# Kernel optimization log

Hardware: AMD Instinct MI355X
Metric: run time of the kernel (lower is better)

Reference implementation:

```python
import jax, jax.numpy as jnp
import numpy as np
from itertools import permutations

N = 4            # n_streams
C = 2048         # hidden_size
NC = N * C
NFACT = 24       # 4!
DFF = 4 * C
B, S = 2, 4096
EPS = 1.1920929e-07  # torch F.rms_norm default eps = finfo(fp32).eps


def _perm_mat():
    perms = list(permutations(range(N)))
    P = np.zeros((len(perms), N * N), np.float32)
    for i, p in enumerate(perms):
        for r, c in enumerate(p):
            P[i, r * N + c] = 1.0
    return jnp.asarray(P)


def setup_inputs() -> dict:
    key = jax.random.key(0)
    ks = jax.random.split(key, 8)
    total_out = 2 * N + NFACT
    return {
        "x_streams": jax.random.normal(ks[0], (B, S, N, C), jnp.float32),
        "W_all": jax.random.normal(ks[1], (total_out, NC), jnp.float32) * (1.0 / np.sqrt(NC)),
        "b_all": jax.random.normal(ks[2], (total_out,), jnp.float32) * 0.02,
        "alpha_pre": jnp.array([0.01], jnp.float32),
        "alpha_post": jnp.array([0.01], jnp.float32),
        "alpha_res": jnp.array([0.01], jnp.float32),
        "W1": jax.random.normal(ks[3], (DFF, C), jnp.float32) * (1.0 / np.sqrt(C)),
        "b1": jnp.zeros((DFF,), jnp.float32),
        "W2": jax.random.normal(ks[4], (C, DFF), jnp.float32) * (1.0 / np.sqrt(DFF)),
        "b2": jnp.zeros((C,), jnp.float32),
        "perm_mat": _perm_mat(),
    }


def reference(x_streams, W_all, b_all, alpha_pre, alpha_post, alpha_res, W1, b1, W2, b2, perm_mat):
    # --- coefficients: fused RMSNorm + projection + gating ---
    x_flat = x_streams.reshape(*x_streams.shape[:-2], NC)            # (B,S,nC)
    x_norm = x_flat * jax.lax.rsqrt(jnp.mean(x_flat * x_flat, axis=-1, keepdims=True) + EPS)
    all_proj = x_norm @ W_all.T                                       # (B,S,2n+n!)
    pre_proj = all_proj[..., :N]
    post_proj = all_proj[..., N:2 * N]
    res_proj = all_proj[..., 2 * N:]
    h_pre = jax.nn.sigmoid(alpha_pre * pre_proj + b_all[:N])          # (B,S,n)
    h_post = 2.0 * jax.nn.sigmoid(alpha_post * post_proj + b_all[N:2 * N])
    a_res = jax.nn.softmax(alpha_res * res_proj + b_all[2 * N:], axis=-1)  # (B,S,n!)
    H_res = (a_res @ perm_mat).reshape(*a_res.shape[:-1], N, N)       # (B,S,n,n)
    H_merged = H_res - h_post[..., :, None] * h_pre[..., None, :]
    # --- pre-map: weighted sum over streams ---
    layer_input = jnp.einsum('bsn,bsnc->bsc', h_pre, x_streams)       # (B,S,C)
    # --- wrapped layer: GELU MLP (no residual) ---
    h = jax.nn.gelu(layer_input @ W1.T + b1, approximate=False)
    layer_output = h @ W2.T + b2                                      # (B,S,C)
    # --- post-res mixing ---
    out = jnp.einsum('bsij,bsjc->bsic', H_merged, x_streams) \
        + h_post[..., None] * layer_output[..., None, :]
    return out
```

## Files before the change

kernel.cpp:

```cpp
#include <hip/hip_runtime.h>
#include <hip/hip_bf16.h>
#include <math.h>

#define NC_DIM 8192
#define C_DIM 2048
#define NTOK 8192
#define EPS_RMS 1.1920929e-07f

typedef __bf16 bf16_t;
typedef __attribute__((ext_vector_type(8))) __bf16 bf16x8;
typedef __attribute__((ext_vector_type(4))) __bf16 bf16x4;
typedef __attribute__((ext_vector_type(4))) float f32x4;

__device__ __forceinline__ void gload_lds16(const void* g, void* l) {
    __builtin_amdgcn_global_load_lds(
        (const __attribute__((address_space(1))) void*)g,
        (__attribute__((address_space(3))) void*)l, 16, 0, 0);
}

__global__ __launch_bounds__(256) void cvt_f32_bf16(const float* __restrict__ in,
                                                    bf16_t* __restrict__ out,
                                                    const int n4) {
    int i = blockIdx.x * 256 + threadIdx.x;
    const int stride = gridDim.x * 256;
    for (; i < n4; i += stride) {
        f32x4 v = ((const f32x4*)in)[i];
        bf16x4 bv;
        bv.x = (__bf16)v.x; bv.y = (__bf16)v.y; bv.z = (__bf16)v.z; bv.w = (__bf16)v.w;
        ((bf16x4*)out)[i] = bv;
    }
}

__global__ __launch_bounds__(256) void k_proj(
    const float* __restrict__ x,
    const float* __restrict__ Wall,
    const float* __restrict__ ball,
    const float* __restrict__ apre,
    const float* __restrict__ apost,
    const float* __restrict__ ares,
    const float* __restrict__ perm,
    float* __restrict__ hpre_g,
    float* __restrict__ hpost_g,
    float* __restrict__ Hm_g)
{
    __shared__ __align__(16) bf16_t xs[32 * 264];
    __shared__ __align__(16) bf16_t wsl[32 * 264];
    __shared__ float dparts[4][32][32];
    __shared__ float ssq_s[32];
    __shared__ float Ps[384];

    const int t = threadIdx.x;
    const int lane = t & 63;
    const int w = t >> 6;
    const int tok0 = blockIdx.x * 32;

    for (int i = t; i < 384; i += 256) Ps[i] = perm[i];

    const int row = t >> 3;
    const int i8 = t & 7;

    const float* xrow = x + (size_t)(tok0 + row) * (size_t)NC_DIM;
    const float* wrow = Wall + (size_t)row * (size_t)NC_DIM;

    float ssq = 0.0f;
    f32x4 acc[2][2];
#pragma unroll
    for (int m = 0; m < 2; ++m)
#pragma unroll
        for (int n = 0; n < 2; ++n) acc[m][n] = (f32x4){0.f, 0.f, 0.f, 0.f};

    const int rsel = lane & 15;
    const int ko_base = (lane >> 4) * 8;

    for (int kt = 0; kt < NC_DIM; kt += 256) {
        __syncthreads();
#pragma unroll
        for (int q = 0; q < 8; ++q) {
            const int col = (i8 + q * 8) * 4;
            f32x4 v = *(const f32x4*)(xrow + kt + col);
            ssq += v.x * v.x + v.y * v.y + v.z * v.z + v.w * v.w;
            bf16x4 bv;
            bv.x = (__bf16)v.x; bv.y = (__bf16)v.y; bv.z = (__bf16)v.z; bv.w = (__bf16)v.w;
            *(bf16x4*)(xs + row * 264 + col) = bv;
            f32x4 u = *(const f32x4*)(wrow + kt + col);
            bf16x4 bu;
            bu.x = (__bf16)u.x; bu.y = (__bf16)u.y; bu.z = (__bf16)u.z; bu.w = (__bf16)u.w;
            *(bf16x4*)(wsl + row * 264 + col) = bu;
        }
        __syncthreads();
#pragma unroll
        for (int ks = 0; ks < 2; ++ks) {
            const int ko = w * 64 + ks * 32 + ko_base;
            bf16x8 a0 = *(const bf16x8*)(xs + rsel * 264 + ko);
            bf16x8 a1 = *(const bf16x8*)(xs + (16 + rsel) * 264 + ko);
            bf16x8 b0 = *(const bf16x8*)(wsl + rsel * 264 + ko);
            bf16x8 b1 = *(const bf16x8*)(wsl + (16 + rsel) * 264 + ko);
            acc[0][0] = __builtin_amdgcn_mfma_f32_16x16x32_bf16(a0, b0, acc[0][0], 0, 0, 0);
            acc[0][1] = __builtin_amdgcn_mfma_f32_16x16x32_bf16(a0, b1, acc[0][1], 0, 0, 0);
            acc[1][0] = __builtin_amdgcn_mfma_f32_16x16x32_bf16(a1, b0, acc[1][0], 0, 0, 0);
            acc[1][1] = __builtin_amdgcn_mfma_f32_16x16x32_bf16(a1, b1, acc[1][1], 0, 0, 0);
        }
    }

    ssq += __shfl_xor(ssq, 1);
    ssq += __shfl_xor(ssq, 2);
    ssq += __shfl_xor(ssq, 4);
    if (i8 == 0) ssq_s[row] = ssq;

    const int cr = (lane >> 4) * 4;
#pragma unroll
    for (int m = 0; m < 2; ++m)
#pragma unroll
        for (int n = 0; n < 2; ++n)
#pragma unroll
            for (int j = 0; j < 4; ++j)
                dparts[w][m * 16 + cr + j][n * 16 + rsel] = acc[m][n][j];
    __syncthreads();

    if (t < 32) {
        const int g = tok0 + t;
        const float rinv = rsqrtf(ssq_s[t] * (1.0f / (float)NC_DIM) + EPS_RMS);
        float proj[32];
#pragma unroll
        for (int r = 0; r < 32; ++r)
            proj[r] = (dparts[0][t][r] + dparts[1][t][r] + dparts[2][t][r] + dparts[3][t][r]) * rinv;
        const float aP = apre[0], aQ = apost[0], aR = ares[0];
        float hp[4], hq[4];
#pragma unroll
        for (int i = 0; i < 4; ++i) {
            hp[i] = 1.0f / (1.0f + expf(-(aP * proj[i] + __ldg(&ball[i]))));
            hq[i] = 2.0f / (1.0f + expf(-(aQ * proj[4 + i] + __ldg(&ball[4 + i]))));
        }
        float zb[24];
        float mx = -1e30f;
#pragma unroll
        for (int p = 0; p < 24; ++p) {
            zb[p] = aR * proj[8 + p] + __ldg(&ball[8 + p]);
            mx = fmaxf(mx, zb[p]);
        }
        float s = 0.f;
#pragma unroll
        for (int p = 0; p < 24; ++p) { zb[p] = expf(zb[p] - mx); s += zb[p]; }
        const float is = 1.0f / s;
        float Hr[16];
#pragma unroll
        for (int idx = 0; idx < 16; ++idx) Hr[idx] = 0.f;
#pragma unroll
        for (int p = 0; p < 24; ++p) {
            const float a = zb[p] * is;
#pragma unroll
            for (int idx = 0; idx < 16; ++idx) Hr[idx] += a * Ps[p * 16 + idx];
        }
#pragma unroll
        for (int i = 0; i < 4; ++i) {
            hpre_g[(size_t)g * 4 + i] = hp[i];
            hpost_g[(size_t)g * 4 + i] = hq[i];
#pragma unroll
            for (int j = 0; j < 4; ++j)
                Hm_g[(size_t)g * 16 + i * 4 + j] = Hr[i * 4 + j] - hq[i] * hp[j];
        }
    }
}

__global__ __launch_bounds__(256) void k_mix(
    const float* __restrict__ x,
    const float* __restrict__ hpre_g,
    bf16_t* __restrict__ li)
{
    __shared__ float hp[8][4];
    const int t = threadIdx.x;
    const size_t tok0 = (size_t)blockIdx.x * 8;
    if (t < 32) hp[t >> 2][t & 3] = hpre_g[tok0 * 4 + t];
    __syncthreads();
    const int tl = t >> 5;
    const int ci = (t & 31) * 4;
    const size_t g = tok0 + tl;
    const float* xb = x + g * (size_t)NC_DIM;
    bf16_t* lo = li + g * (size_t)C_DIM;
    const float h0 = hp[tl][0], h1 = hp[tl][1], h2 = hp[tl][2], h3 = hp[tl][3];
#pragma unroll
    for (int q = 0; q < 16; ++q) {
        const int c = ci + q * 128;
        f32x4 v0 = *(const f32x4*)(xb + c);
        f32x4 v1 = *(const f32x4*)(xb + 2048 + c);
        f32x4 v2 = *(const f32x4*)(xb + 4096 + c);
        f32x4 v3 = *(const f32x4*)(xb + 6144 + c);
        f32x4 r = h0 * v0 + h1 * v1 + h2 * v2 + h3 * v3;
        bf16x4 bv;
        bv.x = (__bf16)r.x; bv.y = (__bf16)r.y; bv.z = (__bf16)r.z; bv.w = (__bf16)r.w;
        *(bf16x4*)(lo + c) = bv;
    }
}

template <int MODE>
__global__ __launch_bounds__(512, 2) void gemm8(
    const bf16_t* __restrict__ A,
    const bf16_t* __restrict__ Bm,
    const float* __restrict__ bias,
    void* __restrict__ Cout,
    const int M, const int N, const int K,
    const float* __restrict__ xg,
    const float* __restrict__ hpost_g,
    const float* __restrict__ Hm_g)
{
    __shared__ __align__(16) char lds[131072];
    const int tid = threadIdx.x;
    const int lane = tid & 63;
    const int w = tid >> 6;
    const int wr = w >> 2;
    const int wc = w & 3;

    const int nbn = N >> 8;
    const int cpx = gridDim.x >> 3;
    const int bid = blockIdx.x;
    const int swz = (bid & 7) * cpx + (bid >> 3);
    const long tm = (long)(swz / nbn) * 256;
    const long tn = (long)(swz % nbn) * 256;

    const int NT = K >> 6;

    const int rsel = lane & 15;
    const int ko = (lane >> 4) * 8;
    const int lane_off = rsel * 64 + ((ko ^ (((rsel >> 1) & 3) << 3)) << 1);

    const char* Abytes = (const char*)A;
    const char* Bbytes = (const char*)Bm;
    size_t asrc[2][2], bsrc[2][2];
#pragma unroll
    for (int i = 0; i < 2; ++i) {
        const int d = i * 8192 + tid * 16;
        {
            const int awr = d >> 13, rem = d & 8191;
            const int sub = rem >> 10, rs = sub >> 1, ksub = sub & 1;
            const int rr = (rem >> 6) & 15;
            const int kk = ((rem & 63) >> 1) ^ (((rr >> 1) & 3) << 3);
            const int k = ksub * 32 + kk;
#pragma unroll
            for (int mq = 0; mq < 2; ++mq) {
                const long grow = tm + awr * 128 + mq * 64 + rs * 16 + rr;
                asrc[mq][i] = ((size_t)grow * K + k) * 2;
            }
        }
        {
            const int bwc = d >> 12, rem = d & 4095;
            const int sub = rem >> 10, rs = sub >> 1, ksub = sub & 1;
            const int rr = (rem >> 6) & 15;
            const int kk = ((rem & 63) >> 1) ^ (((rr >> 1) & 3) << 3);
            const int k = ksub * 32 + kk;
#pragma unroll
            for (int np = 0; np < 2; ++np) {
                const long grow = tn + bwc * 64 + np * 32 + rs * 16 + rr;
                bsrc[np][i] = ((size_t)grow * K + k) * 2;
            }
        }
    }

    auto stageA = [&](int mq, int tile, int slot) {
        const int tt = tile < NT ? tile : NT - 1;
        char* dst = lds + slot * 65536 + mq * 16384 + w * 1024;
        gload_lds16(Abytes + asrc[mq][0] + (size_t)tt * 128, dst);
        gload_lds16(Abytes + asrc[mq][1] + (size_t)tt * 128, dst + 8192);
    };
    auto stageB = [&](int np, int tile, int slot) {
        const int tt = tile < NT ? tile : NT - 1;
        char* dst = lds + slot * 65536 + 32768 + np * 16384 + w * 1024;
        gload_lds16(Bbytes + bsrc[np][0] + (size_t)tt * 128, dst);
        gload_lds16(Bbytes + bsrc[np][1] + (size_t)tt * 128, dst + 8192);
    };

    const char* aB = lds + wr * 8192;
    const char* bB = lds + 32768 + wc * 4096;

    f32x4 acc[8][4];
#pragma unroll
    for (int m = 0; m < 8; ++m)
#pragma unroll
        for (int n = 0; n < 4; ++n) acc[m][n] = (f32x4){0.f, 0.f, 0.f, 0.f};

    bf16x8 aR[4][2], b01[2][2], b23[2][2];

    stageA(0, 0, 0); stageB(0, 0, 0); stageB(1, 0, 0); stageA(1, 0, 0);
    stageA(0, 1, 1); stageB(0, 1, 1); stageB(1, 1, 1);
    asm volatile("s_waitcnt vmcnt(6)" ::: "memory");
    __builtin_amdgcn_s_barrier();

    for (int t = 0; t < NT; ++t) {
        const int s = t & 1;
        const char* aS = aB + s * 65536;
        const char* bS = bB + s * 65536;
#pragma unroll
        for (int mf = 0; mf < 4; ++mf)
#pragma unroll
            for (int ks = 0; ks < 2; ++ks)
                aR[mf][ks] = *(const bf16x8*)(aS + (mf * 2 + ks) * 1024 + lane_off);
#pragma unroll
        for (int nf = 0; nf < 2; ++nf)
#pragma unroll
            for (int ks = 0; ks < 2; ++ks)
                b01[nf][ks] = *(const bf16x8*)(bS + (nf * 2 + ks) * 1024 + lane_off);
        stageA(1, t + 1, s ^ 1);
        __builtin_amdgcn_s_setprio(1);
#pragma unroll
        for (int mf = 0; mf < 4; ++mf)
#pragma unroll
            for (int nf = 0; nf < 2; ++nf)
#pragma unroll
                for (int ks = 0; ks < 2; ++ks)
                    acc[mf][nf] = __builtin_amdgcn_mfma_f32_16x16x32_bf16(aR[mf][ks], b01[nf][ks], acc[mf][nf], 0, 0, 0);
        __builtin_amdgcn_s_setprio(0);
        __builtin_amdgcn_s_barrier();
#pragma unroll
        for (int nf = 0; nf < 2; ++nf)
#pragma unroll
            for (int ks = 0; ks < 2; ++ks)
                b23[nf][ks] = *(const bf16x8*)(bS + 16384 + (nf * 2 + ks) * 1024 + lane_off);
        stageA(0, t + 2, s);
        __builtin_amdgcn_s_setprio(1);
#pragma unroll
        for (int mf = 0; mf < 4; ++mf)
#pragma unroll
            for (int nf = 0; nf < 2; ++nf)
#pragma unroll
                for (int ks = 0; ks < 2; ++ks)
                    acc[mf][2 + nf] = __builtin_amdgcn_mfma_f32_16x16x32_bf16(aR[mf][ks], b23[nf][ks], acc[mf][2 + nf], 0, 0, 0);
        __builtin_amdgcn_s_setprio(0);
        __builtin_amdgcn_s_barrier();
#pragma unroll
        for (int mf = 0; mf < 4; ++mf)
#pragma unroll
            for (int ks = 0; ks < 2; ++ks)
                aR[mf][ks] = *(const bf16x8*)(aS + 16384 + (mf * 2 + ks) * 1024 + lane_off);
        stageB(0, t + 2, s);
        __builtin_amdgcn_s_setprio(1);
#pragma unroll
        for (int mf = 0; mf < 4; ++mf)
#pragma unroll
            for (int nf = 0; nf < 2; ++nf)
#pragma unroll
                for (int ks = 0; ks < 2; ++ks)
                    acc[4 + mf][2 + nf] = __builtin_amdgcn_mfma_f32_16x16x32_bf16(aR[mf][ks], b23[nf][ks], acc[4 + mf][2 + nf], 0, 0, 0);
        __builtin_amdgcn_s_setprio(0);
        __builtin_amdgcn_s_barrier();
        stageB(1, t + 2, s);
        asm volatile("s_waitcnt vmcnt(6)" ::: "memory");
        __builtin_amdgcn_s_setprio(1);
#pragma unroll
        for (int mf = 0; mf < 4; ++mf)
#pragma unroll
            for (int nf = 0; nf < 2; ++nf)
#pragma unroll
                for (int ks = 0; ks < 2; ++ks)
                    acc[4 + mf][nf] = __builtin_amdgcn_mfma_f32_16x16x32_bf16(aR[mf][ks], b01[nf][ks], acc[4 + mf][nf], 0, 0, 0);
        __builtin_amdgcn_s_setprio(0);
        __builtin_amdgcn_s_barrier();
    }

    if (MODE == 0) {
#pragma unroll
        for (int mq = 0; mq < 2; ++mq)
#pragma unroll
            for (int mf = 0; mf < 4; ++mf) {
                const long rbase = tm + wr * 128 + mq * 64 + mf * 16 + (lane >> 4) * 4;
#pragma unroll
                for (int np = 0; np < 2; ++np)
#pragma unroll
                    for (int nf = 0; nf < 2; ++nf) {
                        const long cg = tn + wc * 64 + np * 32 + nf * 16 + rsel;
                        const float bv = __ldg(&bias[cg]);
                        const f32x4 v4 = acc[mq * 4 + mf][np * 2 + nf];
#pragma unroll
                        for (int j = 0; j < 4; ++j) {
                            const float v = v4[j] + bv;
                            const float ge = 0.5f * v * (1.0f + erff(v * 0.70710678118654752f));
                            ((bf16_t*)Cout)[(size_t)(rbase + j) * N + cg] = (__bf16)ge;
                        }
                    }
            }
    } else {
        float* outp = (float*)Cout;
#pragma unroll
        for (int mq = 0; mq < 2; ++mq)
#pragma unroll
            for (int mf = 0; mf < 4; ++mf) {
                const long rbase = tm + wr * 128 + mq * 64 + mf * 16 + (lane >> 4) * 4;
#pragma unroll
                for (int j = 0; j < 4; ++j) {
                    const long tok = rbase + j;
                    float H[16], hq[4];
#pragma unroll
                    for (int z = 0; z < 16; ++z) H[z] = __ldg(&Hm_g[tok * 16 + z]);
#pragma unroll
                    for (int z = 0; z < 4; ++z) hq[z] = __ldg(&hpost_g[tok * 4 + z]);
                    const float* xrow = xg + (size_t)tok * (size_t)NC_DIM;
                    float* orow = outp + (size_t)tok * (size_t)NC_DIM;
#pragma unroll
                    for (int np = 0; np < 2; ++np)
#pragma unroll
                        for (int nf = 0; nf < 2; ++nf) {
                            const long cg = tn + wc * 64 + np * 32 + nf * 16 + rsel;
                            const float lo = acc[mq * 4 + mf][np * 2 + nf][j] + __ldg(&bias[cg]);
                            const float x0 = xrow[cg];
                            const float x1 = xrow[2048 + cg];
                            const float x2 = xrow[4096 + cg];
                            const float x3 = xrow[6144 + cg];
#pragma unroll
                            for (int i = 0; i < 4; ++i)
                                orow[i * 2048 + cg] =
                                    H[i * 4 + 0] * x0 + H[i * 4 + 1] * x1 +
                                    H[i * 4 + 2] * x2 + H[i * 4 + 3] * x3 + hq[i] * lo;
                        }
                }
            }
    }
}

extern "C" void kernel_launch(void* const* d_in, const int* in_sizes, int n_in,
                              void* d_out, int out_size, void* d_ws, size_t ws_size,
                              hipStream_t stream) {
    const float* x     = (const float*)d_in[0];
    const float* Wall  = (const float*)d_in[1];
    const float* ball  = (const float*)d_in[2];
    const float* apre  = (const float*)d_in[3];
    const float* apost = (const float*)d_in[4];
    const float* ares  = (const float*)d_in[5];
    const float* W1    = (const float*)d_in[6];
    const float* b1    = (const float*)d_in[7];
    const float* W2    = (const float*)d_in[8];
    const float* b2    = (const float*)d_in[9];
    const float* perm  = (const float*)d_in[10];
    float* out = (float*)d_out;
    char* ws = (char*)d_ws;

    bf16_t* W1b  = (bf16_t*)(ws);
    bf16_t* W2b  = (bf16_t*)(ws + 33554432ull);
    bf16_t* li   = (bf16_t*)(ws + 67108864ull);
    bf16_t* h    = (bf16_t*)(ws + 100663296ull);
    float*  hpre = (float*)(ws + 301989888ull);
    float*  hpost= (float*)(ws + 302120960ull);
    float*  Hm   = (float*)(ws + 302252032ull);

    cvt_f32_bf16<<<2048, 256, 0, stream>>>(W1, W1b, 16777216 / 4);
    cvt_f32_bf16<<<2048, 256, 0, stream>>>(W2, W2b, 16777216 / 4);
    k_proj<<<256, 256, 0, stream>>>(x, Wall, ball, apre, apost, ares, perm, hpre, hpost, Hm);
    k_mix<<<1024, 256, 0, stream>>>(x, hpre, li);
    gemm8<0><<<1024, 512, 0, stream>>>(li, W1b, b1, (void*)h, 8192, 8192, 2048,
                                       nullptr, nullptr, nullptr);
    gemm8<1><<<256, 512, 0, stream>>>(h, W2b, b2, (void*)out, 8192, 2048, 8192,
                                      x, hpost, Hm);
}
```

Before: 824.9 us.

## Fuse pre-map mixing into projection kernel and retile GEMM block swizzle

The stream-weighted pre-map (k_mix) moves into the projection kernel, which already walks each token row of x, so the separate launch and the hpre round-trip through global memory go away. x is likely re-read from cache while it is still warm. The templated GEMM is split into two specialized kernels that share a new fixed tile swizzle mapping blocks to 4x8 tile groups per XCD, aimed at better L2 reuse. The second GEMM's output stores become nontemporal. The swizzle hardcodes the grid shapes, and the projection kernel now does more serial work on only 256 blocks.

```diff
diff --git a/kernel.cpp b/kernel.cpp
--- a/kernel.cpp
+++ b/kernel.cpp
@@ -16,6 +16,13 @@
     __builtin_amdgcn_global_load_lds(
         (const __attribute__((address_space(1))) void*)g,
         (__attribute__((address_space(3))) void*)l, 16, 0, 0);
+}
+
+__device__ __forceinline__ void tile_swz(int bid, long& tm, long& tn) {
+    const int x8 = bid & 7;
+    const int l = bid >> 3;
+    tm = (long)(x8 * 4 + ((l >> 3) & 3)) * 256;
+    tn = (long)((l >> 5) * 8 + (l & 7)) * 256;
 }
 
 __global__ __launch_bounds__(256) void cvt_f32_bf16(const float* __restrict__ in,
@@ -39,15 +46,16 @@
     const float* __restrict__ apost,
     const float* __restrict__ ares,
     const float* __restrict__ perm,
-    float* __restrict__ hpre_g,
     float* __restrict__ hpost_g,
-    float* __restrict__ Hm_g)
+    float* __restrict__ Hm_g,
+    bf16_t* __restrict__ li)
 {
     __shared__ __align__(16) bf16_t xs[32 * 264];
     __shared__ __align__(16) bf16_t wsl[32 * 264];
     __shared__ float dparts[4][32][32];
     __shared__ float ssq_s[32];
     __shared__ float Ps[384];
+    __shared__ float hps[32][4];
 
     const int t = threadIdx.x;
     const int lane = t & 63;
@@ -130,6 +138,7 @@
         for (int i = 0; i < 4; ++i) {
             hp[i] = 1.0f / (1.0f + expf(-(aP * proj[i] + __ldg(&ball[i]))));
             hq[i] = 2.0f / (1.0f + expf(-(aQ * proj[4 + i] + __ldg(&ball[4 + i]))));
+            hps[t][i] = hp[i];
         }
         float zb[24];
         float mx = -1e30f;
@@ -153,38 +162,23 @@
         }
 #pragma unroll
         for (int i = 0; i < 4; ++i) {
-            hpre_g[(size_t)g * 4 + i] = hp[i];
             hpost_g[(size_t)g * 4 + i] = hq[i];
 #pragma unroll
             for (int j = 0; j < 4; ++j)
                 Hm_g[(size_t)g * 16 + i * 4 + j] = Hr[i * 4 + j] - hq[i] * hp[j];
         }
     }
-}
-
-__global__ __launch_bounds__(256) void k_mix(
-    const float* __restrict__ x,
-    const float* __restrict__ hpre_g,
-    bf16_t* __restrict__ li)
-{
-    __shared__ float hp[8][4];
-    const int t = threadIdx.x;
-    const size_t tok0 = (size_t)blockIdx.x * 8;
-    if (t < 32) hp[t >> 2][t & 3] = hpre_g[tok0 * 4 + t];
     __syncthreads();
-    const int tl = t >> 5;
-    const int ci = (t & 31) * 4;
-    const size_t g = tok0 + tl;
-    const float* xb = x + g * (size_t)NC_DIM;
-    bf16_t* lo = li + g * (size_t)C_DIM;
-    const float h0 = hp[tl][0], h1 = hp[tl][1], h2 = hp[tl][2], h3 = hp[tl][3];
-#pragma unroll
-    for (int q = 0; q < 16; ++q) {
-        const int c = ci + q * 128;
-        f32x4 v0 = *(const f32x4*)(xb + c);
-        f32x4 v1 = *(const f32x4*)(xb + 2048 + c);
-        f32x4 v2 = *(const f32x4*)(xb + 4096 + c);
-        f32x4 v3 = *(const f32x4*)(xb + 6144 + c);
+
+    const float h0 = hps[row][0], h1 = hps[row][1], h2 = hps[row][2], h3 = hps[row][3];
+    bf16_t* lo = li + (size_t)(tok0 + row) * (size_t)C_DIM;
+#pragma unroll 4
+    for (int q = 0; q < 64; ++q) {
+        const int c = (i8 + q * 8) * 4;
+        f32x4 v0 = *(const f32x4*)(xrow + c);
+        f32x4 v1 = *(const f32x4*)(xrow + 2048 + c);
+        f32x4 v2 = *(const f32x4*)(xrow + 4096 + c);
+        f32x4 v3 = *(const f32x4*)(xrow + 6144 + c);
         f32x4 r = h0 * v0 + h1 * v1 + h2 * v2 + h3 * v3;
         bf16x4 bv;
         bv.x = (__bf16)r.x; bv.y = (__bf16)r.y; bv.z = (__bf16)r.z; bv.w = (__bf16)r.w;
@@ -192,16 +186,12 @@
     }
 }
 
-template <int MODE>
-__global__ __launch_bounds__(512, 2) void gemm8(
+__global__ __launch_bounds__(512, 2) void gemm1k(
     const bf16_t* __restrict__ A,
     const bf16_t* __restrict__ Bm,
     const float* __restrict__ bias,
-    void* __restrict__ Cout,
-    const int M, const int N, const int K,
-    const float* __restrict__ xg,
-    const float* __restrict__ hpost_g,
-    const float* __restrict__ Hm_g)
+    bf16_t* __restrict__ Cout,
+    const int M, const int N, const int K)
 {
     __shared__ __align__(16) char lds[131072];
     const int tid = threadIdx.x;
@@ -210,12 +200,8 @@
     const int wr = w >> 2;
     const int wc = w & 3;
 
-    const int nbn = N >> 8;
-    const int cpx = gridDim.x >> 3;
-    const int bid = blockIdx.x;
-    const int swz = (bid & 7) * cpx + (bid >> 3);
-    const long tm = (long)(swz / nbn) * 256;
-    const long tn = (long)(swz % nbn) * 256;
+    long tm, tn;
+    tile_swz(blockIdx.x, tm, tn);
 
     const int NT = K >> 6;
 
@@ -355,63 +341,221 @@
         __builtin_amdgcn_s_barrier();
     }
 
-    if (MODE == 0) {
-#pragma unroll
-        for (int mq = 0; mq < 2; ++mq)
-#pragma unroll
-            for (int mf = 0; mf < 4; ++mf) {
-                const long rbase = tm + wr * 128 + mq * 64 + mf * 16 + (lane >> 4) * 4;
+#pragma unroll
+    for (int mq = 0; mq < 2; ++mq)
+#pragma unroll
+        for (int mf = 0; mf < 4; ++mf) {
+            const long rbase = tm + wr * 128 + mq * 64 + mf * 16 + (lane >> 4) * 4;
+#pragma unroll
+            for (int np = 0; np < 2; ++np)
+#pragma unroll
+                for (int nf = 0; nf < 2; ++nf) {
+                    const long cg = tn + wc * 64 + np * 32 + nf * 16 + rsel;
+                    const float bv = __ldg(&bias[cg]);
+                    const f32x4 v4 = acc[mq * 4 + mf][np * 2 + nf];
+#pragma unroll
+                    for (int j = 0; j < 4; ++j) {
+                        const float v = v4[j] + bv;
+                        const float ge = 0.5f * v * (1.0f + erff(v * 0.70710678118654752f));
+                        Cout[(size_t)(rbase + j) * N + cg] = (__bf16)ge;
+                    }
+                }
+        }
+}
+
+__global__ __launch_bounds__(512, 2) void gemm2f(
+    const bf16_t* __restrict__ A,
+    const bf16_t* __restrict__ Bm,
+    const float* __restrict__ bias,
+    float* __restrict__ outp,
+    const int M, const int N, const int K,
+    const float* __restrict__ xg,
+    const float* __restrict__ hpost_g,
+    const float* __restrict__ Hm_g)
+{
+    __shared__ __align__(16) char lds[131072];
+    const int tid = threadIdx.x;
+    const int lane = tid & 63;
+    const int w = tid >> 6;
+    const int wr = w >> 2;
+    const int wc = w & 3;
+
+    long tm, tn;
+    tile_swz(blockIdx.x, tm, tn);
+
+    const int NT = K >> 6;
+
+    const int rsel = lane & 15;
+    const int ko = (lane >> 4) * 8;
+    const int lane_off = rsel * 64 + ((ko ^ (((rsel >> 1) & 3) << 3)) << 1);
+
+    const char* Abytes = (const char*)A;
+    const char* Bbytes = (const char*)Bm;
+    size_t asrc[2][2], bsrc[2][2];
+#pragma unroll
+    for (int i = 0; i < 2; ++i) {
+        const int d = i * 8192 + tid * 16;
+        {
+            const int awr = d >> 13, rem = d & 8191;
+            const int sub = rem >> 10, rs = sub >> 1, ksub = sub & 1;
+            const int rr = (rem >> 6) & 15;
+            const int kk = ((rem & 63) >> 1) ^ (((rr >> 1) & 3) << 3);
+            const int k = ksub * 32 + kk;
+#pragma unroll
+            for (int mq = 0; mq < 2; ++mq) {
+                const long grow = tm + awr * 128 + mq * 64 + rs * 16 + rr;
+                asrc[mq][i] = ((size_t)grow * K + k) * 2;
+            }
+        }
+        {
+            const int bwc = d >> 12, rem = d & 4095;
+            const int sub = rem >> 10, rs = sub >> 1, ksub = sub & 1;
+            const int rr = (rem >> 6) & 15;
+            const int kk = ((rem & 63) >> 1) ^ (((rr >> 1) & 3) << 3);
+            const int k = ksub * 32 + kk;
+#pragma unroll
+            for (int np = 0; np < 2; ++np) {
+                const long grow = tn + bwc * 64 + np * 32 + rs * 16 + rr;
+                bsrc[np][i] = ((size_t)grow * K + k) * 2;
+            }
+        }
+    }
+
+    auto stageA = [&](int mq, int tile, int slot) {
+        const int tt = tile < NT ? tile : NT - 1;
+        char* dst = lds + slot * 65536 + mq * 16384 + w * 1024;
+        gload_lds16(Abytes + asrc[mq][0] + (size_t)tt * 128, dst);
+        gload_lds16(Abytes + asrc[mq][1] + (size_t)tt * 128, dst + 8192);
+    };
+    auto stageB = [&](int np, int tile, int slot) {
+        const int tt = tile < NT ? tile : NT - 1;
+        char* dst = lds + slot * 65536 + 32768 + np * 16384 + w * 1024;
+        gload_lds16(Bbytes + bsrc[np][0] + (size_t)tt * 128, dst);
+        gload_lds16(Bbytes + bsrc[np][1] + (size_t)tt * 128, dst + 8192);
+    };
+
+    const char* aB = lds + wr * 8192;
+    const char* bB = lds + 32768 + wc * 4096;
+
+    f32x4 acc[8][4];
+#pragma unroll
+    for (int m = 0; m < 8; ++m)
+#pragma unroll
+        for (int n = 0; n < 4; ++n) acc[m][n] = (f32x4){0.f, 0.f, 0.f, 0.f};
+
+    bf16x8 aR[4][2], b01[2][2], b23[2][2];
+
+    stageA(0, 0, 0); stageB(0, 0, 0); stageB(1, 0, 0); stageA(1, 0, 0);
+    stageA(0, 1, 1); stageB(0, 1, 1); stageB(1, 1, 1);
+    asm volatile("s_waitcnt vmcnt(6)" ::: "memory");
+    __builtin_amdgcn_s_barrier();
+
+    for (int t = 0; t < NT; ++t) {
+        const int s = t & 1;
+        const char* aS = aB + s * 65536;
+        const char* bS = bB + s * 65536;
+#pragma unroll
+        for (int mf = 0; mf < 4; ++mf)
+#pragma unroll
+            for (int ks = 0; ks < 2; ++ks)
+                aR[mf][ks] = *(const bf16x8*)(aS + (mf * 2 + ks) * 1024 + lane_off);
+#pragma unroll
+        for (int nf = 0; nf < 2; ++nf)
+#pragma unroll
+            for (int ks = 0; ks < 2; ++ks)
+                b01[nf][ks] = *(const bf16x8*)(bS + (nf * 2 + ks) * 1024 + lane_off);
+        stageA(1, t + 1, s ^ 1);
+        __builtin_amdgcn_s_setprio(1);
+#pragma unroll
+        for (int mf = 0; mf < 4; ++mf)
+#pragma unroll
+            for (int nf = 0; nf < 2; ++nf)
+#pragma unroll
+                for (int ks = 0; ks < 2; ++ks)
+                    acc[mf][nf] = __builtin_amdgcn_mfma_f32_16x16x32_bf16(aR[mf][ks], b01[nf][ks], acc[mf][nf], 0, 0, 0);
+        __builtin_amdgcn_s_setprio(0);
+        __builtin_amdgcn_s_barrier();
+#pragma unroll
+        for (int nf = 0; nf < 2; ++nf)
+#pragma unroll
+            for (int ks = 0; ks < 2; ++ks)
+                b23[nf][ks] = *(const bf16x8*)(bS + 16384 + (nf * 2 + ks) * 1024 + lane_off);
+        stageA(0, t + 2, s);
+        __builtin_amdgcn_s_setprio(1);
+#pragma unroll
+        for (int mf = 0; mf < 4; ++mf)
+#pragma unroll
+            for (int nf = 0; nf < 2; ++nf)
+#pragma unroll
+                for (int ks = 0; ks < 2; ++ks)
+                    acc[mf][2 + nf] = __builtin_amdgcn_mfma_f32_16x16x32_bf16(aR[mf][ks], b23[nf][ks], acc[mf][2 + nf], 0, 0, 0);
+        __builtin_amdgcn_s_setprio(0);
+        __builtin_amdgcn_s_barrier();
+#pragma unroll
+        for (int mf = 0; mf < 4; ++mf)
+#pragma unroll
+            for (int ks = 0; ks < 2; ++ks)
+                aR[mf][ks] = *(const bf16x8*)(aS + 16384 + (mf * 2 + ks) * 1024 + lane_off);
+        stageB(0, t + 2, s);
+        __builtin_amdgcn_s_setprio(1);
+#pragma unroll
+        for (int mf = 0; mf < 4; ++mf)
+#pragma unroll
+            for (int nf = 0; nf < 2; ++nf)
+#pragma unroll
+                for (int ks = 0; ks < 2; ++ks)
+                    acc[4 + mf][2 + nf] = __builtin_amdgcn_mfma_f32_16x16x32_bf16(aR[mf][ks], b23[nf][ks], acc[4 + mf][2 + nf], 0, 0, 0);
+        __builtin_amdgcn_s_setprio(0);
+        __builtin_amdgcn_s_barrier();
+        stageB(1, t + 2, s);
+        asm volatile("s_waitcnt vmcnt(6)" ::: "memory");
+        __builtin_amdgcn_s_setprio(1);
+#pragma unroll
+        for (int mf = 0; mf < 4; ++mf)
+#pragma unroll
+            for (int nf = 0; nf < 2; ++nf)
+#pragma unroll
+                for (int ks = 0; ks < 2; ++ks)
+                    acc[4 + mf][nf] = __builtin_amdgcn_mfma_f32_16x16x32_bf16(aR[mf][ks], b01[nf][ks], acc[4 + mf][nf], 0, 0, 0);
+        __builtin_amdgcn_s_setprio(0);
+        __builtin_amdgcn_s_barrier();
+    }
+
+#pragma unroll
+    for (int mq = 0; mq < 2; ++mq)
+#pragma unroll
+        for (int mf = 0; mf < 4; ++mf) {
+            const long rbase = tm + wr * 128 + mq * 64 + mf * 16 + (lane >> 4) * 4;
+#pragma unroll
+            for (int j = 0; j < 4; ++j) {
+                const long tok = rbase + j;
+                float H[16], hq[4];
+#pragma unroll
+                for (int z = 0; z < 16; ++z) H[z] = __ldg(&Hm_g[tok * 16 + z]);
+#pragma unroll
+                for (int z = 0; z < 4; ++z) hq[z] = __ldg(&hpost_g[tok * 4 + z]);
+                const float* xrow = xg + (size_t)tok * (size_t)NC_DIM;
+                float* orow = outp + (size_t)tok * (size_t)NC_DIM;
 #pragma unroll
                 for (int np = 0; np < 2; ++np)
 #pragma unroll
                     for (int nf = 0; nf < 2; ++nf) {
                         const long cg = tn + wc * 64 + np * 32 + nf * 16 + rsel;
-                        const float bv = __ldg(&bias[cg]);
-                        const f32x4 v4 = acc[mq * 4 + mf][np * 2 + nf];
-#pragma unroll
-                        for (int j = 0; j < 4; ++j) {
-                            const float v = v4[j] + bv;
-                            const float ge = 0.5f * v * (1.0f + erff(v * 0.70710678118654752f));
-                            ((bf16_t*)Cout)[(size_t)(rbase + j) * N + cg] = (__bf16)ge;
+                        const float lo = acc[mq * 4 + mf][np * 2 + nf][j] + __ldg(&bias[cg]);
+                        const float x0 = xrow[cg];
+                        const float x1 = xrow[2048 + cg];
+                        const float x2 = xrow[4096 + cg];
+                        const float x3 = xrow[6144 + cg];
+#pragma unroll
+                        for (int i = 0; i < 4; ++i) {
+                            const float r =
+                                H[i * 4 + 0] * x0 + H[i * 4 + 1] * x1 +
+                                H[i * 4 + 2] * x2 + H[i * 4 + 3] * x3 + hq[i] * lo;
+                            __builtin_nontemporal_store(r, &orow[i * 2048 + cg]);
                         }
                     }
             }
-    } else {
-        float* outp = (float*)Cout;
-#pragma unroll
-        for (int mq = 0; mq < 2; ++mq)
-#pragma unroll
-            for (int mf = 0; mf < 4; ++mf) {
-                const long rbase = tm + wr * 128 + mq * 64 + mf * 16 + (lane >> 4) * 4;
-#pragma unroll
-                for (int j = 0; j < 4; ++j) {
-                    const long tok = rbase + j;
-                    float H[16], hq[4];
-#pragma unroll
-                    for (int z = 0; z < 16; ++z) H[z] = __ldg(&Hm_g[tok * 16 + z]);
-#pragma unroll
-                    for (int z = 0; z < 4; ++z) hq[z] = __ldg(&hpost_g[tok * 4 + z]);
-                    const float* xrow = xg + (size_t)tok * (size_t)NC_DIM;
-                    float* orow = outp + (size_t)tok * (size_t)NC_DIM;
-#pragma unroll
-                    for (int np = 0; np < 2; ++np)
-#pragma unroll
-                        for (int nf = 0; nf < 2; ++nf) {
-                            const long cg = tn + wc * 64 + np * 32 + nf * 16 + rsel;
-                            const float lo = acc[mq * 4 + mf][np * 2 + nf][j] + __ldg(&bias[cg]);
-                            const float x0 = xrow[cg];
-                            const float x1 = xrow[2048 + cg];
-                            const float x2 = xrow[4096 + cg];
-                            const float x3 = xrow[6144 + cg];
-#pragma unroll
-                            for (int i = 0; i < 4; ++i)
-                                orow[i * 2048 + cg] =
-                                    H[i * 4 + 0] * x0 + H[i * 4 + 1] * x1 +
-                                    H[i * 4 + 2] * x2 + H[i * 4 + 3] * x3 + hq[i] * lo;
-                        }
-                }
-            }
-    }
+        }
 }
 
 extern "C" void kernel_launch(void* const* d_in, const int* in_sizes, int n_in,
@@ -435,16 +579,13 @@
     bf16_t* W2b  = (bf16_t*)(ws + 33554432ull);
     bf16_t* li   = (bf16_t*)(ws + 67108864ull);
     bf16_t* h    = (bf16_t*)(ws + 100663296ull);
-    float*  hpre = (float*)(ws + 301989888ull);
     float*  hpost= (float*)(ws + 302120960ull);
     float*  Hm   = (float*)(ws + 302252032ull);
 
     cvt_f32_bf16<<<2048, 256, 0, stream>>>(W1, W1b, 16777216 / 4);
     cvt_f32_bf16<<<2048, 256, 0, stream>>>(W2, W2b, 16777216 / 4);
-    k_proj<<<256, 256, 0, stream>>>(x, Wall, ball, apre, apost, ares, perm, hpre, hpost, Hm);
-    k_mix<<<1024, 256, 0, stream>>>(x, hpre, li);
-    gemm8<0><<<1024, 512, 0, stream>>>(li, W1b, b1, (void*)h, 8192, 8192, 2048,
-                                       nullptr, nullptr, nullptr);
-    gemm8<1><<<256, 512, 0, stream>>>(h, W2b, b2, (void*)out, 8192, 2048, 8192,
-                                      x, hpost, Hm);
-}
+    k_proj<<<256, 256, 0, stream>>>(x, Wall, ball, apre, apost, ares, perm, hpost, Hm, li);
+    gemm1k<<<1024, 512, 0, stream>>>(li, W1b, b1, h, 8192, 8192, 2048);
+    gemm2f<<<256, 512, 0, stream>>>(h, W2b, b2, out, 8192, 2048, 8192,
+                                    x, hpost, Hm);
+}
```

After: 796.6 us. 3.4% less time.
